# Performance work log

Measured on AMD Instinct MI355X. Metric: run time of the kernel, lower is better.

Reference implementation:

```python
import jax, jax.numpy as jnp
import numpy as np

D, HEADS, PTS, NQ, BEV_H, BEV_W, NCLS, BS, NL = 256, 8, 4, 900, 200, 200, 10, 4, 6
HD = D // HEADS
PC = (-51.2, -51.2, -5.0, 51.2, 51.2, 3.0)


def _ln(x, w, b):
    m = x.mean(-1, keepdims=True)
    v = ((x - m) ** 2).mean(-1, keepdims=True)
    return (x - m) * jax.lax.rsqrt(v + 1e-5) * w + b


def _inv_sig(x, eps=1e-5):
    x = jnp.clip(x, 0.0, 1.0)
    return jnp.log(jnp.clip(x, eps, None) / jnp.clip(1.0 - x, eps, None))


def _mha(q_in, k_in, v_in, in_w, in_b, out_w, out_b):
    # torch nn.MultiheadAttention (eval, dropout=0): packed in_proj (3D,D)
    b, n, _ = q_in.shape
    qw, kw, vw = jnp.split(in_w, 3, axis=0)
    qb, kb, vb = jnp.split(in_b, 3, axis=0)
    q = (q_in @ qw.T + qb).reshape(b, n, HEADS, HD)
    k = (k_in @ kw.T + kb).reshape(b, k_in.shape[1], HEADS, HD)
    v = (v_in @ vw.T + vb).reshape(b, v_in.shape[1], HEADS, HD)
    s = jnp.einsum('bqhd,bkhd->bhqk', q, k) * (1.0 / float(np.sqrt(HD)))
    a = jax.nn.softmax(s, axis=-1)
    o = jnp.einsum('bhqk,bkhd->bqhd', a, v).reshape(b, n, D)
    return o @ out_w.T + out_b


def _deform_attn(q, identity, value, ref2d, off_w, off_b, aw_w, aw_b, vp_w, vp_b, op_w, op_b):
    # CustomMSDeformableAttention, num_levels=1, num_points=4; bilinear grid_sample
    # semantics: align_corners=False, zero padding.
    b, n, _ = q.shape
    hw = value.shape[1]
    v = (value @ vp_w.T + vp_b).reshape(b, hw, HEADS, HD)
    vg = v.transpose(0, 2, 1, 3)  # (b, heads, HW, hd)
    off = (q @ off_w.T + off_b).reshape(b, n, HEADS, PTS, 2)
    aw = jax.nn.softmax((q @ aw_w.T + aw_b).reshape(b, n, HEADS, PTS), axis=-1)
    norm = jnp.array([BEV_W, BEV_H], jnp.float32)  # offset_normalizer = (W, H)
    loc = ref2d[:, :, None, None, :] + off / norm  # (b,n,heads,P,2) in [0,1]
    # grid_sample align_corners=False pixel coords
    x = (loc[..., 0] * BEV_W - 0.5).transpose(0, 2, 1, 3)  # (b,heads,n,P)
    y = (loc[..., 1] * BEV_H - 0.5).transpose(0, 2, 1, 3)
    x0 = jnp.floor(x); y0 = jnp.floor(y)
    x0i = x0.astype(jnp.int32); y0i = y0.astype(jnp.int32)
    fx = x - x0; fy = y - y0
    sampled = jnp.zeros(x.shape + (HD,), q.dtype)
    for dy, wy in ((0, 1.0 - fy), (1, fy)):
        for dx, wx in ((0, 1.0 - fx), (1, fx)):
            xi = x0i + dx; yi = y0i + dy
            valid = (xi >= 0) & (xi < BEV_W) & (yi >= 0) & (yi < BEV_H)
            lin = jnp.clip(yi, 0, BEV_H - 1) * BEV_W + jnp.clip(xi, 0, BEV_W - 1)
            g = jnp.take_along_axis(vg, lin.reshape(b, HEADS, n * PTS)[..., None], axis=2)
            g = g.reshape(b, HEADS, n, PTS, HD)
            sampled = sampled + g * (wx * wy * valid)[..., None]
    out = jnp.einsum('bhnpc,bnhp->bnhc', sampled, aw).reshape(b, n, D)
    return identity + (out @ op_w.T + op_b)


def _forward(bev_embed, query_embed, ref_w, ref_b, sa_in_w, sa_in_b, sa_out_w, sa_out_b,
             ln_w, ln_b, off_w, off_b, aw_w, aw_b, vproj_w, vproj_b, oproj_w, oproj_b,
             ffn_w1, ffn_b1, ffn_w2, ffn_b2, reg_w1, reg_b1, reg_w2, reg_b2, reg_w3, reg_b3,
             cls_w1, cls_b1, cls_w2, cls_b2, cls_w3, cls_b3, cls_ln_w, cls_ln_b):
    bs = bev_embed.shape[0]
    qpos = jnp.broadcast_to(query_embed[None, :, :D], (bs, NQ, D))
    q = jnp.broadcast_to(query_embed[None, :, D:], (bs, NQ, D))
    ref = jax.nn.sigmoid(qpos @ ref_w.T + ref_b)  # (bs, NQ, 3)
    init_ref = ref

    def reg_apply(i, x):
        h = jax.nn.relu(x @ reg_w1[i].T + reg_b1[i])
        h = jax.nn.relu(h @ reg_w2[i].T + reg_b2[i])
        return h @ reg_w3[i].T + reg_b3[i]

    hs, refs = [], []
    for i in range(NL):
        # self_attn -> norm
        sa = _mha(q + qpos, q + qpos, q, sa_in_w[i], sa_in_b[i], sa_out_w[i], sa_out_b[i])
        q = _ln(q + sa, ln_w[i, 0], ln_b[i, 0])
        # cross_attn (deformable) -> norm; query_pos added inside attn, identity pre-pos
        ca = _deform_attn(q + qpos, q, bev_embed, ref[..., :2], off_w[i], off_b[i],
                          aw_w[i], aw_b[i], vproj_w[i], vproj_b[i], oproj_w[i], oproj_b[i])
        q = _ln(ca, ln_w[i, 1], ln_b[i, 1])
        # ffn -> norm
        ff = jax.nn.relu(q @ ffn_w1[i].T + ffn_b1[i]) @ ffn_w2[i].T + ffn_b2[i]
        q = _ln(q + ff, ln_w[i, 2], ln_b[i, 2])
        # iterative box refinement (detached in torch)
        tmp = reg_apply(i, q)
        new_ref = jnp.concatenate([
            jax.nn.sigmoid(tmp[..., :2] + _inv_sig(ref[..., :2])),
            jax.nn.sigmoid(tmp[..., 4:5] + _inv_sig(ref[..., 2:3]))], axis=-1)
        ref = jax.lax.stop_gradient(new_ref)
        hs.append(q)
        refs.append(ref)

    cls_list, coord_list = [], []
    for i in range(NL):
        r = _inv_sig(init_ref if i == 0 else refs[i - 1])
        x = hs[i]
        h = jax.nn.relu(_ln(x @ cls_w1[i].T + cls_b1[i], cls_ln_w[i, 0], cls_ln_b[i, 0]))
        h = jax.nn.relu(_ln(h @ cls_w2[i].T + cls_b2[i], cls_ln_w[i, 1], cls_ln_b[i, 1]))
        cls = h @ cls_w3[i].T + cls_b3[i]
        tmp = reg_apply(i, x)
        xy = jax.nn.sigmoid(tmp[..., 0:2] + r[..., 0:2])
        z = jax.nn.sigmoid(tmp[..., 4:5] + r[..., 2:3])
        cx = xy[..., 0:1] * (PC[3] - PC[0]) + PC[0]
        cy = xy[..., 1:2] * (PC[4] - PC[1]) + PC[1]
        cz = z * (PC[5] - PC[2]) + PC[2]
        coord = jnp.concatenate([cx, cy, tmp[..., 2:4], cz, tmp[..., 5:]], axis=-1)
        cls_list.append(cls)
        coord_list.append(coord)
    # (NL, bs, NQ, NCLS+10): classes and boxes concatenated on last dim
    return jnp.concatenate([jnp.stack(cls_list), jnp.stack(coord_list)], axis=-1)


def setup_inputs() -> dict:
    key = jax.random.key(0)
    ks = iter(jax.random.split(key, 64))
    def nrm(shape, s=0.02):
        return jax.random.normal(next(ks), shape, jnp.float32) * s
    d, C = D, NCLS
    return dict(
        bev_embed=jax.random.normal(next(ks), (BS, BEV_H * BEV_W, d), jnp.float32),
        query_embed=nrm((NQ, 2 * d), 1.0),
        ref_w=nrm((3, d)), ref_b=jnp.zeros((3,), jnp.float32),
        sa_in_w=nrm((NL, 3 * d, d)), sa_in_b=jnp.zeros((NL, 3 * d), jnp.float32),
        sa_out_w=nrm((NL, d, d)), sa_out_b=jnp.zeros((NL, d), jnp.float32),
        ln_w=jnp.ones((NL, 3, d), jnp.float32), ln_b=jnp.zeros((NL, 3, d), jnp.float32),
        off_w=nrm((NL, HEADS * PTS * 2, d)), off_b=nrm((NL, HEADS * PTS * 2), 0.5),
        aw_w=nrm((NL, HEADS * PTS, d)), aw_b=jnp.zeros((NL, HEADS * PTS), jnp.float32),
        vproj_w=nrm((NL, d, d)), vproj_b=jnp.zeros((NL, d), jnp.float32),
        oproj_w=nrm((NL, d, d)), oproj_b=jnp.zeros((NL, d), jnp.float32),
        ffn_w1=nrm((NL, 2 * d, d)), ffn_b1=jnp.zeros((NL, 2 * d), jnp.float32),
        ffn_w2=nrm((NL, d, 2 * d)), ffn_b2=jnp.zeros((NL, d), jnp.float32),
        reg_w1=nrm((NL, d, d)), reg_b1=jnp.zeros((NL, d), jnp.float32),
        reg_w2=nrm((NL, d, d)), reg_b2=jnp.zeros((NL, d), jnp.float32),
        reg_w3=nrm((NL, 10, d)), reg_b3=jnp.zeros((NL, 10), jnp.float32),
        cls_w1=nrm((NL, d, d)), cls_b1=jnp.zeros((NL, d), jnp.float32),
        cls_w2=nrm((NL, d, d)), cls_b2=jnp.zeros((NL, d), jnp.float32),
        cls_w3=nrm((NL, C, d)), cls_b3=jnp.zeros((NL, C), jnp.float32),
        cls_ln_w=jnp.ones((NL, 2, d), jnp.float32), cls_ln_b=jnp.zeros((NL, 2, d), jnp.float32),
    )


def reference(bev_embed, query_embed, ref_w, ref_b, sa_in_w, sa_in_b, sa_out_w, sa_out_b,
              ln_w, ln_b, off_w, off_b, aw_w, aw_b, vproj_w, vproj_b, oproj_w, oproj_b,
              ffn_w1, ffn_b1, ffn_w2, ffn_b2, reg_w1, reg_b1, reg_w2, reg_b2, reg_w3, reg_b3,
              cls_w1, cls_b1, cls_w2, cls_b2, cls_w3, cls_b3, cls_ln_w, cls_ln_b):
    return _forward(bev_embed, query_embed, ref_w, ref_b, sa_in_w, sa_in_b, sa_out_w, sa_out_b,
                    ln_w, ln_b, off_w, off_b, aw_w, aw_b, vproj_w, vproj_b, oproj_w, oproj_b,
                    ffn_w1, ffn_b1, ffn_w2, ffn_b2, reg_w1, reg_b1, reg_w2, reg_b2, reg_w3, reg_b3,
                    cls_w1, cls_b1, cls_w2, cls_b2, cls_w3, cls_b3, cls_ln_w, cls_ln_b)
```

## Files before the change

kernel.cpp:

```cpp
#include <hip/hip_runtime.h>
#include <math.h>

#define DD 256
#define NQQ 900
#define NBS 4
#define NLAYER 6
#define BEVH 200
#define BEVW 200
#define ROWS (NBS*NQQ)
#define BIGN (1<<30)
#define KDEF 2080

typedef __attribute__((ext_vector_type(8))) short bf16x8;
typedef __attribute__((ext_vector_type(4))) float f32x4;

__device__ __forceinline__ float sigmoidf_(float x){ return 1.0f/(1.0f+expf(-x)); }
__device__ __forceinline__ float invsigf_(float x){
  x = fminf(fmaxf(x,0.0f),1.0f);
  float lo = fmaxf(x,1e-5f), hi = fmaxf(1.0f-x,1e-5f);
  return logf(lo/hi);
}
__device__ __forceinline__ unsigned f2bf1(float x){
  unsigned u = __float_as_uint(x);
  return (u + 0x7fffu + ((u>>16)&1u)) >> 16;
// ... 153 lines not shown
    for (int fr=0; fr<2; ++fr)
      #pragma unroll
      for (int fc=0; fc<2; ++fc) {
        const f32x4 av = fr ? (fc ? acc11 : acc10) : (fc ? acc01 : acc00);
        const int col = n0 + wc*32 + fc*16 + fm;
        const float bias = (col<N) ? ((col<NB) ? B0[col] : B1[col-NB]) : 0.0f;
        #pragma unroll
        for (int r=0; r<4; ++r)
          writeout(av[r] + bias, m0 + wr*32 + fr*16 + kb*4 + r, col);
      }
  } else {
    const int ai0 = fm*32 + ((kb^(fm&3))<<3);
    const int ai1 = (fm+16)*32 + ((kb^(fm&3))<<3);
    const int bcol = wv*16 + fm;
    const int bi = bcol*32 + ((kb^(bcol&3))<<3);
    f32x4 acc0={0,0,0,0}, acc1={0,0,0,0};
    loadg(0); writes(0); __syncthreads();
    for (int s=0; s<NS; ++s) {
      if (s+1<NS) loadg((s+1)<<5);
      const int bf = s&1;
      bf16x8 a0 = *(bf16x8*)&As[bf][ai0];
      bf16x8 a1 = *(bf16x8*)&As[bf][ai1];
      bf16x8 b  = *(bf16x8*)&Bs[bf][bi];
      acc0 = __builtin_amdgcn_mfma_f32_16x16x32_bf16(a0,b,acc0,0,0,0);
      acc1 = __builtin_amdgcn_mfma_f32_16x16x32_bf16(a1,b,acc1,0,0,0);
      if (s+1<NS) { __syncthreads(); writes((s+1)&1); __syncthreads(); }
    }
    const int col = n0 + wv*16 + fm;
    const float bias = (col<N) ? ((col<NB) ? B0[col] : B1[col-NB]) : 0.0f;
    #pragma unroll
    for (int r=0; r<4; ++r) {
      writeout(acc0[r] + bias, m0 + kb*4 + r, col);
      writeout(acc1[r] + bias, m0 + 16 + kb*4 + r, col);
    }
  }
}

__global__ __launch_bounds__(256) void attn3_k(
    const ushort* __restrict__ QKb, const ushort* __restrict__ Vb, ushort* __restrict__ Ob)
{
  const int b = blockIdx.x >> 3, h = blockIdx.x & 7;
  const int wv = threadIdx.x >> 6, lane = threadIdx.x & 63;
  const int t = threadIdx.x;
  const int qt = blockIdx.y*64 + wv*16;
  const int lq = lane & 15, lg = lane >> 4;
  const int q = qt + lq;

  __shared__ ushort Ks[2][32*40];
  __shared__ ushort Vt[2][32*34];

  bf16x8 qf = *(const bf16x8*)(QKb + (size_t)(b*NQQ + min(q, NQQ-1))*512 + h*32 + lg*8);
  f32x4 ot0 = {0.f,0.f,0.f,0.f}, ot1 = {0.f,0.f,0.f,0.f};
  float m = -3e38f, l = 0.0f;

  const ushort* kg = QKb + (size_t)b*NQQ*512 + 256 + h*32;
  const ushort* vg = Vb  + (size_t)b*NQQ*256 + h*32;
  const int srow = t>>3, sc4 = (t&7)*4;

  ushort4 kv, vv;
  auto sload = [&](int k0){
    const int gr = min(k0 + srow, NQQ-1);
    kv = *(const ushort4*)(kg + (size_t)gr*512 + sc4);
    vv = *(const ushort4*)(vg + (size_t)gr*256 + sc4);
  };
  auto swrite = [&](int bf){
    *(ushort4*)&Ks[bf][srow*40 + sc4] = kv;
    Vt[bf][(sc4+0)*34 + srow] = vv.x;
    Vt[bf][(sc4+1)*34 + srow] = vv.y;
    Vt[bf][(sc4+2)*34 + srow] = vv.z;
    Vt[bf][(sc4+3)*34 + srow] = vv.w;
// ... 48 lines not shown
    const int A1 = __builtin_amdgcn_ds_bpermute(pbase,    c01);
    const int B1 = __builtin_amdgcn_ds_bpermute(pbase,    c11);
    const int A2 = __builtin_amdgcn_ds_bpermute(pbase+64, c00);
    const int B2 = __builtin_amdgcn_ds_bpermute(pbase+64, c10);
    const int A3 = __builtin_amdgcn_ds_bpermute(pbase+64, c01);
    const int B3 = __builtin_amdgcn_ds_bpermute(pbase+64, c11);
    union { bf16x8 v; int u[4]; } pv;
    pv.u[0] = hiC ? B0 : A0; pv.u[1] = hiC ? B1 : A1;
    pv.u[2] = hiC ? B2 : A2; pv.u[3] = hiC ? B3 : A3;

    bf16x8 vf0, vf1;
    {
      union { bf16x8 v; unsigned u[4]; } u0, u1;
      const int rb = 8*lg;
      #pragma unroll
      for (int jj=0;jj<4;++jj) {
        u0.u[jj] = *(const unsigned*)&Vt[bf][lq*34 + rb + 2*jj];
        u1.u[jj] = *(const unsigned*)&Vt[bf][(16+lq)*34 + rb + 2*jj];
      }
      vf0 = u0.v; vf1 = u1.v;
    }
    ot0 = __builtin_amdgcn_mfma_f32_16x16x32_bf16(vf0, pv.v, ot0, 0, 0, 0);
    ot1 = __builtin_amdgcn_mfma_f32_16x16x32_bf16(vf1, pv.v, ot1, 0, 0, 0);
    if (c+1 < NC) { __syncthreads(); swrite((c+1)&1); __syncthreads(); }
  }
  if (q < NQQ && qt < NQQ) {
    const float inv = 1.0f / l;
    ushort* op = Ob + (size_t)(b*NQQ + q)*256 + h*32;
    uint2 w0, w1;
    w0.x = pk2(ot0[0]*inv, ot0[1]*inv); w0.y = pk2(ot0[2]*inv, ot0[3]*inv);
    w1.x = pk2(ot1[0]*inv, ot1[1]*inv); w1.y = pk2(ot1[2]*inv, ot1[3]*inv);
    *(uint2*)(op + 4*lg)      = w0;
    *(uint2*)(op + 16 + 4*lg) = w1;
  }
}

__global__ __launch_bounds__(256) void ln_k(
    const float* X, int xld, const float* R,
    const float* __restrict__ w, const float* __restrict__ b,
    float* Y, ushort* Yb, const float* qpos, ushort* Ypb, int relu)
{
  const int row = blockIdx.x*4 + (threadIdx.x>>6);
  const int lane = threadIdx.x & 63;
  if (row >= ROWS) return;
  float4 x = *(const float4*)(X + (size_t)row*xld + (lane<<2));
  if (R) { const float4 r = *(const float4*)(R + (size_t)row*256 + (lane<<2)); x.x+=r.x; x.y+=r.y; x.z+=r.z; x.w+=r.w; }
  float s = x.x+x.y+x.z+x.w;
  #pragma unroll
  for (int o=32;o>0;o>>=1) s += __shfl_xor(s,o);
  const float mean = s * (1.0f/256.0f);
  float4 d; d.x=x.x-mean; d.y=x.y-mean; d.z=x.z-mean; d.w=x.w-mean;
  float s2 = d.x*d.x+d.y*d.y+d.z*d.z+d.w*d.w;
  #pragma unroll
  for (int o=32;o>0;o>>=1) s2 += __shfl_xor(s2,o);
  const float rs = rsqrtf(s2*(1.0f/256.0f) + 1e-5f);
  const float4 wv = *(const float4*)(w + (lane<<2));
  const float4 bv = *(const float4*)(b + (lane<<2));
  float4 y;
  y.x = d.x*rs*wv.x + bv.x; y.y = d.y*rs*wv.y + bv.y;
  y.z = d.z*rs*wv.z + bv.z; y.w = d.w*rs*wv.w + bv.w;
  if (relu) { y.x=fmaxf(y.x,0.f); y.y=fmaxf(y.y,0.f); y.z=fmaxf(y.z,0.f); y.w=fmaxf(y.w,0.f); }
  if (Y)  *(float4*)(Y + (size_t)row*256 + (lane<<2)) = y;
  if (Yb) *(ushort4*)(Yb + (size_t)row*256 + (lane<<2)) = pk4(y);
  if (Ypb) {
    const float4 qp = *(const float4*)(qpos + (size_t)row*256 + (lane<<2));
    float4 zz; zz.x=y.x+qp.x; zz.y=y.y+qp.y; zz.z=y.z+qp.z; zz.w=y.w+qp.w;
    *(ushort4*)(Ypb + (size_t)row*256 + (lane<<2)) = pk4(zz);
  }
}

__global__ __launch_bounds__(512) void gather_k(
    const ushort* __restrict__ bevb, const float* __restrict__ offaw,
    const float* __restrict__ ref, ushort* __restrict__ rr)
{
  const int row = blockIdx.x;
  const int h = threadIdx.x >> 6, lane = threadIdx.x & 63;
  const int b = row / NQQ;
  const float refx = ref[row*3+0], refy = ref[row*3+1];
  const float* oa = offaw + (size_t)row*96;
  float aw[4];
  {
    const float a0=oa[64+h*4+0], a1=oa[64+h*4+1], a2=oa[64+h*4+2], a3=oa[64+h*4+3];
    const float mx = fmaxf(fmaxf(a0,a1), fmaxf(a2,a3));
    const float e0=__expf(a0-mx), e1=__expf(a1-mx), e2=__expf(a2-mx), e3=__expf(a3-mx);
    const float inv = 1.0f/(e0+e1+e2+e3);
    aw[0]=e0*inv; aw[1]=e1*inv; aw[2]=e2*inv; aw[3]=e3*inv;
  }
  float r0=0.f, r1=0.f, r2=0.f, r3=0.f, sacc=0.f;
  const ushort* bb = bevb + (size_t)b*BEVH*BEVW*DD;
  #pragma unroll
  for (int p=0;p<4;++p) {
    const float ox = oa[h*8+p*2+0], oy = oa[h*8+p*2+1];
    const float x = (refx + ox*(1.0f/BEVW))*BEVW - 0.5f;
    const float y = (refy + oy*(1.0f/BEVH))*BEVH - 0.5f;
    const float x0f = floorf(x), y0f = floorf(y);
    const int x0 = (int)x0f, y0 = (int)y0f;
    const float fx = x - x0f, fy = y - y0f;
    #pragma unroll
    for (int dy=0;dy<2;++dy) {
      #pragma unroll
// ... 36 lines not shown
  }
  __syncthreads();
  const int tx = t&15, ty = t>>4;
  float acc[4][4] = {};
  for (int j=0;j<32;++j) {
    float a[4], bv[4];
    #pragma unroll
    for (int r=0;r<4;++r) a[r] = Ao[ty*4+r][j];
    #pragma unroll
    for (int cc=0;cc<4;++cc) bv[cc] = Bo[j][tx*4+cc];
    #pragma unroll
    for (int r=0;r<4;++r)
      #pragma unroll
      for (int cc=0;cc<4;++cc) acc[r][cc] += a[r]*bv[cc];
  }
  #pragma unroll
  for (int r=0;r<4;++r)
    #pragma unroll
    for (int cc=0;cc<4;++cc)
      Wfull[((size_t)l*256 + ct*64+ty*4+r)*KDEF + h*256 + kt*64 + tx*4+cc] = (ushort)f2bf1(acc[r][cc]);
}

__global__ void wcombB_k(const float* __restrict__ opw, const float* __restrict__ vpb,
                         ushort* __restrict__ Wfull)
{
  const int l = blockIdx.x; const int c = threadIdx.x;
  ushort* wr = Wfull + ((size_t)l*256 + c)*KDEF;
  for (int h=0; h<8; ++h) {
    float s = 0.f;
    for (int j=0;j<32;++j) s += opw[(size_t)l*65536 + (size_t)c*256 + h*32+j] * vpb[l*256 + h*32+j];
    wr[2048 + h] = (ushort)f2bf1(s);
  }
  for (int zz=2056; zz<KDEF; ++zz) wr[zz] = 0;
}

__global__ __launch_bounds__(256) void regcls3_k(
    const float* __restrict__ rc2,
    const float* __restrict__ lnw, const float* __restrict__ lnb,
    const float* __restrict__ rw3, const float* __restrict__ rb3,
    const float* __restrict__ cw3, const float* __restrict__ cb3,
    float* __restrict__ ref, float* __restrict__ outL)
{
  __shared__ float Wr[10*272];
  __shared__ float Wc[10*272];
  for (int i=threadIdx.x; i<2560; i+=256) {
    const int o = i>>8, k = i&255;
    const int si = o*272 + (k>>6)*68 + (k&63);
    Wr[si] = rw3[i]; Wc[si] = cw3[i];
  }
  __syncthreads();
  const int t = threadIdx.x;
  const int row = t>>3, g = (t>>2)&1, sl = t&3;
  const int R = blockIdx.x*32 + row;
  const bool act = R < ROWS;
  const float* base = rc2 + (size_t)(act?R:0)*512 + g*256 + sl*64;
  float4 v[16];
  #pragma unroll
  for (int jj=0;jj<16;++jj) v[jj] = *(const float4*)(base + 4*jj);
  float s1 = 0.f, s2 = 0.f;
  #pragma unroll
  for (int jj=0;jj<16;++jj) {
    s1 += v[jj].x+v[jj].y+v[jj].z+v[jj].w;
    s2 += v[jj].x*v[jj].x+v[jj].y*v[jj].y+v[jj].z*v[jj].z+v[jj].w*v[jj].w;
  }
  s1 += __shfl_xor(s1,1); s1 += __shfl_xor(s1,2);
  s2 += __shfl_xor(s2,1); s2 += __shfl_xor(s2,2);
  if (g) {
    const float mean = s1*(1.0f/256.0f);
    const float var = s2*(1.0f/256.0f) - mean*mean;
    const float rs = rsqrtf(var + 1e-5f);
    #pragma unroll
    for (int jj=0;jj<16;++jj) {
      const float4 w4 = *(const float4*)(lnw + sl*64 + 4*jj);
      const float4 b4 = *(const float4*)(lnb + sl*64 + 4*jj);
      v[jj].x = fmaxf((v[jj].x-mean)*rs*w4.x + b4.x, 0.f);
      v[jj].y = fmaxf((v[jj].y-mean)*rs*w4.y + b4.y, 0.f);
      v[jj].z = fmaxf((v[jj].z-mean)*rs*w4.z + b4.z, 0.f);
      v[jj].w = fmaxf((v[jj].w-mean)*rs*w4.w + b4.w, 0.f);
    }
  }
  const float* Wg = g ? Wc : Wr;
  float acc[10] = {};
  #pragma unroll
  for (int jj=0;jj<16;++jj) {
    #pragma unroll
    for (int o=0;o<10;++o) {
      const float4 w = *(const float4*)&Wg[o*272 + sl*68 + 4*jj];
      acc[o] += v[jj].x*w.x + v[jj].y*w.y + v[jj].z*w.z + v[jj].w*w.w;
    }
  }
  #pragma unroll
  for (int o=0;o<10;++o) {
    acc[o] += __shfl_xor(acc[o], 1);
    acc[o] += __shfl_xor(acc[o], 2);
  }
  if (act && sl == 0) {
    if (g) {
      float* oc = outL + (size_t)R*20;
      #pragma unroll
      for (int o=0;o<10;++o) oc[o] = acc[o] + cb3[o];
    } else {
      float tt[10];
      #pragma unroll
      for (int o=0;o<10;++o) tt[o] = acc[o] + rb3[o];
      const float rx = invsigf_(ref[R*3+0]);
      const float ry = invsigf_(ref[R*3+1]);
      const float rz = invsigf_(ref[R*3+2]);
      const float nx = sigmoidf_(tt[0]+rx);
      const float ny = sigmoidf_(tt[1]+ry);
      const float nz = sigmoidf_(tt[4]+rz);
      ref[R*3+0]=nx; ref[R*3+1]=ny; ref[R*3+2]=nz;
      float* o = outL + (size_t)R*20 + 10;
      o[0]=nx*102.4f-51.2f; o[1]=ny*102.4f-51.2f; o[2]=tt[2]; o[3]=tt[3];
      o[4]=nz*8.0f-5.0f; o[5]=tt[5]; o[6]=tt[6]; o[7]=tt[7]; o[8]=tt[8]; o[9]=tt[9];
    }
  }
}

__global__ void init_k(const float* __restrict__ qe, float* __restrict__ qpos,
                       float* __restrict__ q, ushort* __restrict__ qb, ushort* __restrict__ qpb)
{
  const int t = blockIdx.x*blockDim.x + threadIdx.x;
  const int row = t >> 6; const int cc = (t & 63) << 2;
  const int n = row % NQQ;
  const float4 vp = *(const float4*)(qe + (size_t)n*512 + cc);
  const float4 vq = *(const float4*)(qe + (size_t)n*512 + 256 + cc);
  *(float4*)(qpos + (size_t)row*256 + cc) = vp;
  *(float4*)(q    + (size_t)row*256 + cc) = vq;
  *(ushort4*)(qb  + (size_t)row*256 + cc) = pk4(vq);
  float4 s; s.x=vq.x+vp.x; s.y=vq.y+vp.y; s.z=vq.z+vp.z; s.w=vq.w+vp.w;
  *(ushort4*)(qpb + (size_t)row*256 + cc) = pk4(s);
}

__global__ void prep_k(const float* __restrict__ ow, const float* __restrict__ ob,
                       const float* __restrict__ aw, const float* __restrict__ ab,
                       const float* __restrict__ rw, const float* __restrict__ rb,
                       const float* __restrict__ cw, const float* __restrict__ cb,
                       ushort* cwAb, float* cbA, ushort* cwBb, float* cbB)
{
  const int i = blockIdx.x*blockDim.x + threadIdx.x;
  if (i < 6*96*256) {
    const int l = i/(96*256), r = (i/256)%96, k = i%256;
    const float v = (r<64) ? ow[((size_t)l*64 + r)*256 + k] : aw[((size_t)l*32 + (r-64))*256 + k];
    cwAb[i] = (ushort)f2bf1(v);
  }
  if (i < 576) { const int l = i/96, r = i%96; cbA[i] = (r<64) ? ob[l*64+r] : ab[l*32 + r-64]; }
  if (i < 6*512*256) {
    const int l = i/(512*256), r = (i/256)%512, k = i%256;
    const float v = (r<256) ? rw[((size_t)l*256+r)*256+k] : cw[((size_t)l*256 + (r-256))*256 + k];
// ... 59 lines not shown
  const float* reg_w1   = (const float*)d_in[22];
  const float* reg_b1   = (const float*)d_in[23];
  const float* reg_w2   = (const float*)d_in[24];
  const float* reg_b2   = (const float*)d_in[25];
  const float* reg_w3   = (const float*)d_in[26];
  const float* reg_b3   = (const float*)d_in[27];
  const float* cls_w1   = (const float*)d_in[28];
  const float* cls_b1   = (const float*)d_in[29];
  const float* cls_w2   = (const float*)d_in[30];
  const float* cls_b2   = (const float*)d_in[31];
  const float* cls_w3   = (const float*)d_in[32];
  const float* cls_b3   = (const float*)d_in[33];
  const float* cls_ln_w = (const float*)d_in[34];
  const float* cls_ln_b = (const float*)d_in[35];
  float* out = (float*)d_out;

  float* ws    = (float*)d_ws;
  float* qpos  = ws;
  float* q     = qpos + 921600;
  float* tA    = q    + 921600;
  float* tB    = tA   + 921600;
  float* rc2   = tB   + 921600;
  float* cls1f = rc2  + 1843200;
  float* offaw = cls1f+ 921600;
  float* ref   = offaw+ 345600;
  float* cbA   = ref  + 10800;
  float* cbB   = cbA  + 576;
  ushort* usb  = (ushort*)(ws + 6811248);
  ushort* rr   = usb;
  ushort* QKb  = usb;
  ushort* Vb   = usb + 1843200;
  ushort* tAb  = usb + 2764800;
  ushort* W5b  = usb + 3686400;
  ushort* clsb = usb + 5529600;
  ushort* regb = usb + 6451200;
  ushort* qb   = usb + 7488000;
  ushort* qpb  = usb + 8409600;
  ushort* bevb = usb + 9331200;
  ushort* wbf  = usb + 50291200;
  ushort* siwb = wbf;
  ushort* sowb = wbf + 1179648;
  ushort* f1wb = wbf + 1966080;
  ushort* f2wb = wbf + 2752512;
  ushort* r2wb = wbf + 3538944;
  ushort* c2wb = wbf + 3932160;
  ushort* cwAb = wbf + 4325376;
  ushort* cwBb = wbf + 4472832;
  ushort* Wfull= wbf + 5259264;

  auto G = [&](int BM, const ushort* A0, const ushort* A1, int NA, int lda,
               const ushort* W0, const ushort* W1, int NW,
               const float* B0, const float* B1, int NB,
               void* Y0, int ldy0, int obf0,
               void* Y1, int ldy1, int obf1, int NY,
               int M, int N, int K, int reluN) {
    dim3 grid((M+BM-1)/BM, (N+63)/64);
    if (BM==64)
      gemmb_k<64><<<grid, 256, 0, stream>>>(A0,A1,NA,lda,W0,W1,NW,B0,B1,NB,
                                            Y0,ldy0,obf0,Y1,ldy1,obf1,NY,M,N,K,reluN);
    else
      gemmb_k<32><<<grid, 256, 0, stream>>>(A0,A1,NA,lda,W0,W1,NW,B0,B1,NB,
                                            Y0,ldy0,obf0,Y1,ldy1,obf1,NY,M,N,K,reluN);
  };

  cvtbev_k<<<20000, 256, 0, stream>>>(bev, bevb);
  cvtw_k<<<4224, 256, 0, stream>>>(sa_in_w, sa_out_w, oproj_w, ffn_w1, ffn_w2, reg_w2, cls_w2, wbf);
  prep_k<<<3072, 256, 0, stream>>>(off_w, off_b, aw_w, aw_b, reg_w1, reg_b1, cls_w1, cls_b1,
                                   cwAb, cbA, cwBb, cbB);
  wcomb_k<<<dim3(16,8,6), 256, 0, stream>>>(oproj_w, vproj_w, Wfull);
  wcombB_k<<<6, 256, 0, stream>>>(oproj_w, vproj_b, Wfull);
  init_k<<<900, 256, 0, stream>>>(qe, qpos, q, qb, qpb);
  {
    dim3 grid((ROWS+63)/64, 1);
    gemm_k<<<grid, 256, 0, stream>>>(qpos, 256, ref_w, ref_b, ref, ROWS, 3, 256, 3, 2);
  }

  for (int i=0;i<NLAYER;++i) {
    const float* sib = sa_in_b + (size_t)i*768;
    const ushort* siw = siwb + (size_t)i*196608;
    G(64, qpb, qb, 512, 256, siw, siw, BIGN, sib, sib, BIGN,
      QKb, 512, 1, Vb, 256, 1, 512, ROWS, 768, 256, 0);
    attn3_k<<<dim3(32,15), 256, 0, stream>>>(QKb, Vb, tAb);
    G(32, tAb, tAb, BIGN, 256, sowb + (size_t)i*65536, nullptr, BIGN,
      sa_out_b + (size_t)i*256, nullptr, BIGN,
      tB, 256, 0, nullptr, 0, 0, BIGN, ROWS, 256, 256, 0);
    ln_k<<<900, 256, 0, stream>>>(tB, 256, q, ln_w + (size_t)(i*3+0)*256, ln_b + (size_t)(i*3+0)*256,
                                  q, nullptr, qpos, qpb, 0);
    G(32, qpb, qpb, BIGN, 256, cwAb + (size_t)i*24576, nullptr, BIGN,
      cbA + i*96, nullptr, BIGN,
      offaw, 96, 0, nullptr, 0, 0, BIGN, ROWS, 96, 256, 0);
    gather_k<<<ROWS, 512, 0, stream>>>(bevb, offaw, ref, rr);
    G(32, rr, rr, BIGN, KDEF, Wfull + (size_t)i*256*KDEF, nullptr, BIGN,
      oproj_b + (size_t)i*256, nullptr, BIGN,
      tA, 256, 0, nullptr, 0, 0, BIGN, ROWS, 256, KDEF, 0);
    ln_k<<<900, 256, 0, stream>>>(tA, 256, q, ln_w + (size_t)(i*3+1)*256, ln_b + (size_t)(i*3+1)*256,
                                  q, qb, nullptr, nullptr, 0);
    G(64, qb, qb, BIGN, 256, f1wb + (size_t)i*131072, nullptr, BIGN,
      ffn_b1 + (size_t)i*512, nullptr, BIGN,
      W5b, 512, 1, nullptr, 0, 0, BIGN, ROWS, 512, 256, 512);
    G(32, W5b, W5b, BIGN, 512, f2wb + (size_t)i*131072, nullptr, BIGN,
      ffn_b2 + (size_t)i*256, nullptr, BIGN,
      tA, 256, 0, nullptr, 0, 0, BIGN, ROWS, 256, 512, 0);
    ln_k<<<900, 256, 0, stream>>>(tA, 256, q, ln_w + (size_t)(i*3+2)*256, ln_b + (size_t)(i*3+2)*256,
                                  q, qb, qpos, qpb, 0);
    G(64, qb, qb, BIGN, 256, cwBb + (size_t)i*131072, nullptr, BIGN,
      cbB + i*512, nullptr, BIGN,
      regb, 256, 1, cls1f, 256, 0, 256, ROWS, 512, 256, 256);
    ln_k<<<900, 256, 0, stream>>>(cls1f, 256, nullptr,
                                  cls_ln_w + (size_t)(i*2+0)*256, cls_ln_b + (size_t)(i*2+0)*256,
                                  nullptr, clsb, nullptr, nullptr, 1);
    G(64, regb, clsb, 256, 256,
      r2wb + (size_t)i*65536, c2wb + (size_t)i*65536, 256,
      reg_b2 + (size_t)i*256, cls_b2 + (size_t)i*256, 256,
      rc2, 512, 0, nullptr, 0, 0, BIGN, ROWS, 512, 256, 256);
    regcls3_k<<<(ROWS+31)/32, 256, 0, stream>>>(rc2,
        cls_ln_w + (size_t)(i*2+1)*256, cls_ln_b + (size_t)(i*2+1)*256,
        reg_w3 + (size_t)i*2560, reg_b3 + (size_t)i*10,
        cls_w3 + (size_t)i*2560, cls_b3 + (size_t)i*10,
        ref, out + (size_t)i*ROWS*20);
  }
}
```

Before: 1.169 ms.

## Fuse output GEMMs with residual-add LayerNorm in full-row kernels

Adds a templated fullrow_k kernel. Each block computes all output columns for 16 rows with bf16 MFMA, staging the accumulators in shared memory. It then applies bias, residual add, LayerNorm and optional ReLU, and writes the fp32, bf16 and bf16+qpos outputs directly. This replaces four GEMM + ln_k pairs per layer, which removes the separate LN launches and the fp32 intermediate round trips. In exchange, only 225 blocks are launched and every block streams the whole weight matrix, including the K=2080 deformable projection, so weight traffic per block rises and parallelism drops. Variance is now computed as E[x²]−mean², which is less numerically stable than the old two-pass form.

Measured after the change: 1.262 ms. 8.0% more time.

```diff
diff --git a/kernel.cpp b/kernel.cpp
--- a/kernel.cpp
+++ b/kernel.cpp
@@ -213,6 +213,155 @@
   }
 }
 
+template<int BN, int MODE>
+__global__ __launch_bounds__(256) void fullrow_k(
+    const ushort* __restrict__ A, int lda, const ushort* __restrict__ W,
+    const float* __restrict__ bias,
+    const float* __restrict__ R, const float* __restrict__ lnw, const float* __restrict__ lnb,
+    float* __restrict__ Yq, ushort* __restrict__ Yb,
+    const float* __restrict__ qpos, ushort* __restrict__ Ypb,
+    ushort* __restrict__ regb, ushort* __restrict__ clsb, int K)
+{
+  constexpr int P   = (MODE==0) ? 260 : 516;
+  constexpr int SMG = BN*64 + 1024;
+  constexpr int SME = 16*P*4;
+  constexpr int SMB = (SMG > SME) ? SMG : SME;
+  __shared__ char smraw[SMB];
+  ushort* Ws = (ushort*)smraw;
+  ushort* As = ((ushort*)smraw) + BN*32;
+  float*  Ep = (float*)smraw;
+
+  const int t = threadIdx.x;
+  const int m0 = blockIdx.x*16;
+  const int wv = t>>6, lane = t&63;
+  const int fm = lane&15, kb = lane>>4;
+  constexpr int NF = BN/64;
+  constexpr int WR = BN/256;
+  const int colbase = wv*(BN/4);
+  const int NS = K>>5;
+
+  const int arow = t>>2, ak = t&3;
+  const ushort* ap = A + (size_t)(m0+arow)*lda + ak*8;
+
+  bf16x8 pa; bf16x8 pw[WR*4];
+  auto loadr = [&](int c){
+    if (t < 64) pa = *(const bf16x8*)(ap + c*32);
+    #pragma unroll
+    for (int rr2=0; rr2<WR; ++rr2) {
+      const ushort* wp = W + (size_t)(t + rr2*256)*K + c*32;
+      #pragma unroll
+      for (int j=0;j<4;++j) pw[rr2*4+j] = *(const bf16x8*)(wp + j*8);
+    }
+  };
+  auto stores = [&](){
+    if (t < 64) *(bf16x8*)&As[arow*32 + ((ak ^ (arow&3))<<3)] = pa;
+    #pragma unroll
+    for (int rr2=0; rr2<WR; ++rr2) {
+      const int wr = t + rr2*256;
+      #pragma unroll
+      for (int j=0;j<4;++j)
+        *(bf16x8*)&Ws[wr*32 + ((j ^ (wr&3))<<3)] = pw[rr2*4+j];
+    }
+  };
+
+  f32x4 acc[NF];
+  #pragma unroll
+  for (int f=0;f<NF;++f) acc[f] = (f32x4){0,0,0,0};
+
+  loadr(0); stores(); __syncthreads();
+  for (int s=0; s<NS; ++s) {
+    if (s+1<NS) loadr(s+1);
+    bf16x8 af = *(bf16x8*)&As[fm*32 + ((kb ^ (fm&3))<<3)];
+    #pragma unroll
+    for (int f=0;f<NF;++f) {
+      const int col = colbase + f*16 + fm;
+      bf16x8 bfv = *(bf16x8*)&Ws[col*32 + ((kb ^ (col&3))<<3)];
+      acc[f] = __builtin_amdgcn_mfma_f32_16x16x32_bf16(af, bfv, acc[f], 0, 0, 0);
+    }
+    __syncthreads();
+    if (s+1<NS) { stores(); __syncthreads(); }
+  }
+
+  #pragma unroll
+  for (int f=0;f<NF;++f) {
+    const int col = colbase + f*16 + fm;
+    const float bs = bias[col];
+    #pragma unroll
+    for (int r=0;r<4;++r) Ep[(kb*4+r)*P + col] = acc[f][r] + bs;
+  }
+  __syncthreads();
+
+  const int row = t>>4, cg = t&15;
+  const int gr = m0 + row;
+  if constexpr (MODE==0) {
+    float x[16];
+    float s1 = 0.f, s2 = 0.f;
+    const float* rp = R + (size_t)gr*256 + cg*16;
+    #pragma unroll
+    for (int j=0;j<16;j+=4) {
+      float4 e = *(float4*)&Ep[row*P + cg*16 + j];
+      const float4 rv = *(const float4*)(rp + j);
+      x[j]=e.x+rv.x; x[j+1]=e.y+rv.y; x[j+2]=e.z+rv.z; x[j+3]=e.w+rv.w;
+      s1 += x[j]+x[j+1]+x[j+2]+x[j+3];
+      s2 += x[j]*x[j]+x[j+1]*x[j+1]+x[j+2]*x[j+2]+x[j+3]*x[j+3];
+    }
+    s1 += __shfl_xor(s1,1); s1 += __shfl_xor(s1,2); s1 += __shfl_xor(s1,4); s1 += __shfl_xor(s1,8);
+    s2 += __shfl_xor(s2,1); s2 += __shfl_xor(s2,2); s2 += __shfl_xor(s2,4); s2 += __shfl_xor(s2,8);
+    const float mean = s1*(1.0f/256.0f);
+    const float var  = s2*(1.0f/256.0f) - mean*mean;
+    const float rs   = rsqrtf(var + 1e-5f);
+    #pragma unroll
+    for (int j=0;j<16;j+=4) {
+      const float4 w4 = *(const float4*)(lnw + cg*16 + j);
+      const float4 b4 = *(const float4*)(lnb + cg*16 + j);
+      float4 y;
+      y.x = (x[j+0]-mean)*rs*w4.x + b4.x;
+      y.y = (x[j+1]-mean)*rs*w4.y + b4.y;
+      y.z = (x[j+2]-mean)*rs*w4.z + b4.z;
+      y.w = (x[j+3]-mean)*rs*w4.w + b4.w;
+      *(float4*)&Yq[(size_t)gr*256 + cg*16 + j] = y;
+      if (Yb) *(ushort4*)&Yb[(size_t)gr*256 + cg*16 + j] = pk4(y);
+      if (Ypb) {
+        const float4 qp = *(const float4*)(qpos + (size_t)gr*256 + cg*16 + j);
+        float4 z; z.x=y.x+qp.x; z.y=y.y+qp.y; z.z=y.z+qp.z; z.w=y.w+qp.w;
+        *(ushort4*)&Ypb[(size_t)gr*256 + cg*16 + j] = pk4(z);
+      }
+    }
+  } else {
+    #pragma unroll
+    for (int j=0;j<16;j+=4) {
+      float4 e = *(float4*)&Ep[row*P + cg*16 + j];
+      e.x=fmaxf(e.x,0.f); e.y=fmaxf(e.y,0.f); e.z=fmaxf(e.z,0.f); e.w=fmaxf(e.w,0.f);
+      *(ushort4*)&regb[(size_t)gr*256 + cg*16 + j] = pk4(e);
+    }
+    float x[16];
+    float s1 = 0.f, s2 = 0.f;
+    #pragma unroll
+    for (int j=0;j<16;j+=4) {
+      const float4 e = *(float4*)&Ep[row*P + 256 + cg*16 + j];
+      x[j]=e.x; x[j+1]=e.y; x[j+2]=e.z; x[j+3]=e.w;
+      s1 += e.x+e.y+e.z+e.w;
+      s2 += e.x*e.x+e.y*e.y+e.z*e.z+e.w*e.w;
+    }
+    s1 += __shfl_xor(s1,1); s1 += __shfl_xor(s1,2); s1 += __shfl_xor(s1,4); s1 += __shfl_xor(s1,8);
+    s2 += __shfl_xor(s2,1); s2 += __shfl_xor(s2,2); s2 += __shfl_xor(s2,4); s2 += __shfl_xor(s2,8);
+    const float mean = s1*(1.0f/256.0f);
+    const float var  = s2*(1.0f/256.0f) - mean*mean;
+    const float rs   = rsqrtf(var + 1e-5f);
+    #pragma unroll
+    for (int j=0;j<16;j+=4) {
+      const float4 w4 = *(const float4*)(lnw + cg*16 + j);
+      const float4 b4 = *(const float4*)(lnb + cg*16 + j);
+      float4 y;
+      y.x = fmaxf((x[j+0]-mean)*rs*w4.x + b4.x, 0.f);
+      y.y = fmaxf((x[j+1]-mean)*rs*w4.y + b4.y, 0.f);
+      y.z = fmaxf((x[j+2]-mean)*rs*w4.z + b4.z, 0.f);
+      y.w = fmaxf((x[j+3]-mean)*rs*w4.w + b4.w, 0.f);
+      *(ushort4*)&clsb[(size_t)gr*256 + cg*16 + j] = pk4(y);
+    }
+  }
+}
+
 __global__ __launch_bounds__(256) void attn3_k(
     const ushort* __restrict__ QKb, const ushort* __restrict__ Vb, ushort* __restrict__ Ob)
 {
@@ -327,40 +476,6 @@
     w1.x = pk2(ot1[0]*inv, ot1[1]*inv); w1.y = pk2(ot1[2]*inv, ot1[3]*inv);
     *(uint2*)(op + 4*lg)      = w0;
     *(uint2*)(op + 16 + 4*lg) = w1;
-  }
-}
-
-__global__ __launch_bounds__(256) void ln_k(
-    const float* X, int xld, const float* R,
-    const float* __restrict__ w, const float* __restrict__ b,
-    float* Y, ushort* Yb, const float* qpos, ushort* Ypb, int relu)
-{
-  const int row = blockIdx.x*4 + (threadIdx.x>>6);
-  const int lane = threadIdx.x & 63;
-  if (row >= ROWS) return;
-  float4 x = *(const float4*)(X + (size_t)row*xld + (lane<<2));
-  if (R) { const float4 r = *(const float4*)(R + (size_t)row*256 + (lane<<2)); x.x+=r.x; x.y+=r.y; x.z+=r.z; x.w+=r.w; }
-  float s = x.x+x.y+x.z+x.w;
-  #pragma unroll
-  for (int o=32;o>0;o>>=1) s += __shfl_xor(s,o);
-  const float mean = s * (1.0f/256.0f);
-  float4 d; d.x=x.x-mean; d.y=x.y-mean; d.z=x.z-mean; d.w=x.w-mean;
-  float s2 = d.x*d.x+d.y*d.y+d.z*d.z+d.w*d.w;
-  #pragma unroll
-  for (int o=32;o>0;o>>=1) s2 += __shfl_xor(s2,o);
-  const float rs = rsqrtf(s2*(1.0f/256.0f) + 1e-5f);
-  const float4 wv = *(const float4*)(w + (lane<<2));
-  const float4 bv = *(const float4*)(b + (lane<<2));
-  float4 y;
-  y.x = d.x*rs*wv.x + bv.x; y.y = d.y*rs*wv.y + bv.y;
-  y.z = d.z*rs*wv.z + bv.z; y.w = d.w*rs*wv.w + bv.w;
-  if (relu) { y.x=fmaxf(y.x,0.f); y.y=fmaxf(y.y,0.f); y.z=fmaxf(y.z,0.f); y.w=fmaxf(y.w,0.f); }
-  if (Y)  *(float4*)(Y + (size_t)row*256 + (lane<<2)) = y;
-  if (Yb) *(ushort4*)(Yb + (size_t)row*256 + (lane<<2)) = pk4(y);
-  if (Ypb) {
-    const float4 qp = *(const float4*)(qpos + (size_t)row*256 + (lane<<2));
-    float4 zz; zz.x=y.x+qp.x; zz.y=y.y+qp.y; zz.z=y.z+qp.z; zz.w=y.w+qp.w;
-    *(ushort4*)(Ypb + (size_t)row*256 + (lane<<2)) = pk4(zz);
   }
 }
 
@@ -720,34 +835,29 @@
     G(64, qpb, qb, 512, 256, siw, siw, BIGN, sib, sib, BIGN,
       QKb, 512, 1, Vb, 256, 1, 512, ROWS, 768, 256, 0);
     attn3_k<<<dim3(32,15), 256, 0, stream>>>(QKb, Vb, tAb);
-    G(32, tAb, tAb, BIGN, 256, sowb + (size_t)i*65536, nullptr, BIGN,
-      sa_out_b + (size_t)i*256, nullptr, BIGN,
-      tB, 256, 0, nullptr, 0, 0, BIGN, ROWS, 256, 256, 0);
-    ln_k<<<900, 256, 0, stream>>>(tB, 256, q, ln_w + (size_t)(i*3+0)*256, ln_b + (size_t)(i*3+0)*256,
-                                  q, nullptr, qpos, qpb, 0);
+    fullrow_k<256,0><<<225, 256, 0, stream>>>(
+        tAb, 256, sowb + (size_t)i*65536, sa_out_b + (size_t)i*256,
+        q, ln_w + (size_t)(i*3+0)*256, ln_b + (size_t)(i*3+0)*256,
+        q, nullptr, qpos, qpb, nullptr, nullptr, 256);
     G(32, qpb, qpb, BIGN, 256, cwAb + (size_t)i*24576, nullptr, BIGN,
       cbA + i*96, nullptr, BIGN,
       offaw, 96, 0, nullptr, 0, 0, BIGN, ROWS, 96, 256, 0);
     gather_k<<<ROWS, 512, 0, stream>>>(bevb, offaw, ref, rr);
-    G(32, rr, rr, BIGN, KDEF, Wfull + (size_t)i*256*KDEF, nullptr, BIGN,
-      oproj_b + (size_t)i*256, nullptr, BIGN,
-      tA, 256, 0, nullptr, 0, 0, BIGN, ROWS, 256, KDEF, 0);
-    ln_k<<<900, 256, 0, stream>>>(tA, 256, q, ln_w + (size_t)(i*3+1)*256, ln_b + (size_t)(i*3+1)*256,
-                                  q, qb, nullptr, nullptr, 0);
+    fullrow_k<256,0><<<225, 256, 0, stream>>>(
+        rr, KDEF, Wfull + (size_t)i*256*KDEF, oproj_b + (size_t)i*256,
+        q, ln_w + (size_t)(i*3+1)*256, ln_b + (size_t)(i*3+1)*256,
+        q, qb, nullptr, nullptr, nullptr, nullptr, KDEF);
     G(64, qb, qb, BIGN, 256, f1wb + (size_t)i*131072, nullptr, BIGN,
       ffn_b1 + (size_t)i*512, nullptr, BIGN,
       W5b, 512, 1, nullptr, 0, 0, BIGN, ROWS, 512, 256, 512);
-    G(32, W5b, W5b, BIGN, 512, f2wb + (size_t)i*131072, nullptr, BIGN,
-      ffn_b2 + (size_t)i*256, nullptr, BIGN,
-      tA, 256, 0, nullptr, 0, 0, BIGN, ROWS, 256, 512, 0);
-    ln_k<<<900, 256, 0, stream>>>(tA, 256, q, ln_w + (size_t)(i*3+2)*256, ln_b + (size_t)(i*3+2)*256,
-                                  q, qb, qpos, qpb, 0);
-    G(64, qb, qb, BIGN, 256, cwBb + (size_t)i*131072, nullptr, BIGN,
-      cbB + i*512, nullptr, BIGN,
-      regb, 256, 1, cls1f, 256, 0, 256, ROWS, 512, 256, 256);
-    ln_k<<<900, 256, 0, stream>>>(cls1f, 256, nullptr,
-                                  cls_ln_w + (size_t)(i*2+0)*256, cls_ln_b + (size_t)(i*2+0)*256,
-                                  nullptr, clsb, nullptr, nullptr, 1);
+    fullrow_k<256,0><<<225, 256, 0, stream>>>(
+        W5b, 512, f2wb + (size_t)i*131072, ffn_b2 + (size_t)i*256,
+        q, ln_w + (size_t)(i*3+2)*256, ln_b + (size_t)(i*3+2)*256,
+        q, qb, qpos, qpb, nullptr, nullptr, 512);
+    fullrow_k<512,1><<<225, 256, 0, stream>>>(
+        qb, 256, cwBb + (size_t)i*131072, cbB + i*512,
+        nullptr, cls_ln_w + (size_t)(i*2+0)*256, cls_ln_b + (size_t)(i*2+0)*256,
+        nullptr, nullptr, nullptr, nullptr, regb, clsb, 256);
     G(64, regb, clsb, 256, 256,
       r2wb + (size_t)i*65536, c2wb + (size_t)i*65536, 256,
       reg_b2 + (size_t)i*256, cls_b2 + (size_t)i*256, 256,
```

## Fuse reg/cls branch MLP heads and final projection into one tail kernel

Applied to the files above, without the earlier changes.

Replaces the per-layer sequence of two GEMM launches, a LayerNorm launch and the regcls3 kernel with a single tail_k that processes 16 rows per block. The first layer, ReLU or LayerNorm+ReLU, the second layer and the final 10-wide projections with reference-point update all run in shared memory. This removes three launches per layer and the global round trips of regb, clsb, cls1f and rc2. In exchange only 225 blocks of 16 rows are launched, and each block re-streams the full weight matrices from global through a small shared tile with many syncs, which may underuse the MFMA units and the GPU's compute units.

Measured after the change: 1.339 ms. 14.6% more time.

```diff
diff --git a/kernel.cpp b/kernel.cpp
--- a/kernel.cpp
+++ b/kernel.cpp
@@ -209,6 +209,217 @@
     for (int r=0; r<4; ++r) {
       writeout(acc0[r] + bias, m0 + kb*4 + r, col);
       writeout(acc1[r] + bias, m0 + 16 + kb*4 + r, col);
+    }
+  }
+}
+
+__global__ __launch_bounds__(256) void tail_k(
+    const ushort* __restrict__ qb,
+    const ushort* __restrict__ w1, const float* __restrict__ b1,
+    const float* __restrict__ ln1w, const float* __restrict__ ln1b,
+    const ushort* __restrict__ w2r, const ushort* __restrict__ w2c,
+    const float* __restrict__ b2r, const float* __restrict__ b2c,
+    const float* __restrict__ ln2w, const float* __restrict__ ln2b,
+    const float* __restrict__ rw3, const float* __restrict__ rb3,
+    const float* __restrict__ cw3, const float* __restrict__ cb3,
+    float* __restrict__ ref, float* __restrict__ outL)
+{
+  __shared__ ushort As_[16*264];
+  __shared__ ushort Ws_[64*128];
+  __shared__ ushort Ar_[16*256];
+  __shared__ ushort Ac_[16*256];
+  __shared__ float  Hc_[16*264];
+
+  const int t = threadIdx.x;
+  const int m0 = blockIdx.x*16;
+  const int wv = t>>6, lane = t&63;
+  const int fm = lane&15, kb = lane>>4;
+  const int colL = wv*16 + fm;
+
+  {
+    const int row = t>>4, seg = t&15;
+    const ushort* ap = qb + (size_t)(m0+row)*256 + seg*16;
+    #pragma unroll
+    for (int j=0;j<2;++j) {
+      bf16x8 v = *(const bf16x8*)(ap + j*8);
+      const int k = seg*16 + j*8;
+      *(bf16x8*)&As_[row*264 + ((k>>5)<<5) + ((((k>>3)&3)^(row&3))<<3)] = v;
+    }
+  }
+  __syncthreads();
+
+  for (int chunk=0; chunk<8; ++chunk) {
+    f32x4 acc = {0,0,0,0};
+    for (int kc=0; kc<2; ++kc) {
+      __syncthreads();
+      for (int i=t; i<1024; i+=256) {
+        const int r = i>>4, kl = (i&15)*8;
+        bf16x8 v = *(const bf16x8*)(w1 + (size_t)(chunk*64+r)*256 + kc*128 + kl);
+        *(bf16x8*)&Ws_[r*128 + ((kl>>5)<<5) + ((((kl>>3)&3)^(r&3))<<3)] = v;
+      }
+      __syncthreads();
+      #pragma unroll
+      for (int s=0;s<4;++s) {
+        const int st = kc*4 + s;
+        bf16x8 af  = *(bf16x8*)&As_[fm*264 + (st<<5) + ((kb^(fm&3))<<3)];
+        bf16x8 bfv = *(bf16x8*)&Ws_[colL*128 + (s<<5) + ((kb^(colL&3))<<3)];
+        acc = __builtin_amdgcn_mfma_f32_16x16x32_bf16(af, bfv, acc, 0,0,0);
+      }
+    }
+    const int gcol = chunk*64 + colL;
+    const float bias = b1[gcol];
+    #pragma unroll
+    for (int r=0;r<4;++r) {
+      const int row = kb*4 + r;
+      float v = acc[r] + bias;
+      if (chunk < 4) {
+        v = fmaxf(v, 0.0f);
+        Ar_[row*256 + ((gcol>>5)<<5) + ((((gcol>>3)&3)^(row&3))<<3) + (gcol&7)] = (ushort)f2bf1(v);
+      } else {
+        Hc_[row*264 + (gcol-256)] = v;
+      }
+    }
+  }
+  __syncthreads();
+
+  {
+    const int row = t>>4, cg = t&15;
+    float x[16]; float s1=0.f, s2=0.f;
+    #pragma unroll
+    for (int j=0;j<16;j+=4) {
+      float4 e = *(float4*)&Hc_[row*264 + cg*16 + j];
+      x[j]=e.x; x[j+1]=e.y; x[j+2]=e.z; x[j+3]=e.w;
+      s1 += e.x+e.y+e.z+e.w;
+      s2 += e.x*e.x+e.y*e.y+e.z*e.z+e.w*e.w;
+    }
+    s1 += __shfl_xor(s1,1); s1 += __shfl_xor(s1,2); s1 += __shfl_xor(s1,4); s1 += __shfl_xor(s1,8);
+    s2 += __shfl_xor(s2,1); s2 += __shfl_xor(s2,2); s2 += __shfl_xor(s2,4); s2 += __shfl_xor(s2,8);
+    const float mean = s1*(1.0f/256.0f);
+    const float var  = s2*(1.0f/256.0f) - mean*mean;
+    const float rs   = rsqrtf(var + 1e-5f);
+    #pragma unroll
+    for (int jj=0;jj<2;++jj) {
+      const int k0 = cg*16 + jj*8;
+      union { bf16x8 v; unsigned u[4]; } uu;
+      #pragma unroll
+      for (int p=0;p<4;++p) {
+        const int j = jj*8 + p*2;
+        const float w0 = ln1w[k0 + p*2],     b0 = ln1b[k0 + p*2];
+        const float w1v = ln1w[k0 + p*2 + 1], b1v = ln1b[k0 + p*2 + 1];
+        const float y0 = fmaxf((x[j]-mean)*rs*w0 + b0, 0.0f);
+        const float y1 = fmaxf((x[j+1]-mean)*rs*w1v + b1v, 0.0f);
+        uu.u[p] = pk2(y0, y1);
+      }
+      *(bf16x8*)&Ac_[row*256 + ((k0>>5)<<5) + ((((k0>>3)&3)^(row&3))<<3)] = uu.v;
+    }
+  }
+  __syncthreads();
+
+  for (int chunk=0; chunk<8; ++chunk) {
+    const ushort* Wsrc = (chunk<4) ? w2r : w2c;
+    const int wrb = (chunk&3)*64;
+    f32x4 acc = {0,0,0,0};
+    for (int kc=0; kc<2; ++kc) {
+      __syncthreads();
+      for (int i=t; i<1024; i+=256) {
+        const int r = i>>4, kl = (i&15)*8;
+        bf16x8 v = *(const bf16x8*)(Wsrc + (size_t)(wrb+r)*256 + kc*128 + kl);
+        *(bf16x8*)&Ws_[r*128 + ((kl>>5)<<5) + ((((kl>>3)&3)^(r&3))<<3)] = v;
+      }
+      __syncthreads();
+      #pragma unroll
+      for (int s=0;s<4;++s) {
+        const int st = kc*4 + s;
+        const ushort* Asrc = (chunk<4) ? Ar_ : Ac_;
+        bf16x8 af  = *(bf16x8*)&Asrc[fm*256 + (st<<5) + ((kb^(fm&3))<<3)];
+        bf16x8 bfv = *(bf16x8*)&Ws_[colL*128 + (s<<5) + ((kb^(colL&3))<<3)];
+        acc = __builtin_amdgcn_mfma_f32_16x16x32_bf16(af, bfv, acc, 0,0,0);
+      }
+    }
+    const int gcol2 = wrb + colL;
+    const float bias = (chunk<4) ? b2r[gcol2] : b2c[gcol2];
+    #pragma unroll
+    for (int r=0;r<4;++r) {
+      const int row = kb*4 + r;
+      float v = acc[r] + bias;
+      if (chunk < 4) {
+        v = fmaxf(v, 0.0f);
+        As_[row*264 + gcol2] = (ushort)f2bf1(v);
+      } else {
+        Hc_[row*264 + gcol2] = v;
+      }
+    }
+  }
+  __syncthreads();
+
+  {
+    const int row = t>>4, sub = t&15;
+    const int g = sub>>3, sl = sub&7;
+    const int R = m0 + row;
+    float x[32];
+    if (g == 0) {
+      #pragma unroll
+      for (int j=0;j<32;j+=4) {
+        ushort4 u = *(ushort4*)&As_[row*264 + sl*32 + j];
+        x[j]=bf2f(u.x); x[j+1]=bf2f(u.y); x[j+2]=bf2f(u.z); x[j+3]=bf2f(u.w);
+      }
+    } else {
+      float s1=0.f, s2=0.f;
+      #pragma unroll
+      for (int j=0;j<32;j+=4) {
+        float4 e = *(float4*)&Hc_[row*264 + sl*32 + j];
+        x[j]=e.x; x[j+1]=e.y; x[j+2]=e.z; x[j+3]=e.w;
+        s1 += e.x+e.y+e.z+e.w;
+        s2 += e.x*e.x+e.y*e.y+e.z*e.z+e.w*e.w;
+      }
+      s1 += __shfl_xor(s1,1); s1 += __shfl_xor(s1,2); s1 += __shfl_xor(s1,4);
+      s2 += __shfl_xor(s2,1); s2 += __shfl_xor(s2,2); s2 += __shfl_xor(s2,4);
+      const float mean = s1*(1.0f/256.0f);
+      const float var  = s2*(1.0f/256.0f) - mean*mean;
+      const float rs   = rsqrtf(var + 1e-5f);
+      #pragma unroll
+      for (int j=0;j<32;++j) {
+        const int k = sl*32 + j;
+        x[j] = fmaxf((x[j]-mean)*rs*ln2w[k] + ln2b[k], 0.0f);
+      }
+    }
+    const float* W3 = g ? cw3 : rw3;
+    float acc[10] = {};
+    #pragma unroll
+    for (int o=0;o<10;++o) {
+      const float* wp = W3 + o*256 + sl*32;
+      #pragma unroll
+      for (int j=0;j<32;j+=4) {
+        const float4 w = *(const float4*)(wp + j);
+        acc[o] += x[j]*w.x + x[j+1]*w.y + x[j+2]*w.z + x[j+3]*w.w;
+      }
+    }
+    #pragma unroll
+    for (int o=0;o<10;++o) {
+      acc[o] += __shfl_xor(acc[o],1);
+      acc[o] += __shfl_xor(acc[o],2);
+      acc[o] += __shfl_xor(acc[o],4);
+    }
+    if (sl == 0) {
+      if (g) {
+        float* oc = outL + (size_t)R*20;
+        #pragma unroll
+        for (int o=0;o<10;++o) oc[o] = acc[o] + cb3[o];
+      } else {
+        float tt[10];
+        #pragma unroll
+        for (int o=0;o<10;++o) tt[o] = acc[o] + rb3[o];
+        const float rx = invsigf_(ref[R*3+0]);
+        const float ry = invsigf_(ref[R*3+1]);
+        const float rz = invsigf_(ref[R*3+2]);
+        const float nx = sigmoidf_(tt[0]+rx);
+        const float ny = sigmoidf_(tt[1]+ry);
+        const float nz = sigmoidf_(tt[4]+rz);
+        ref[R*3+0]=nx; ref[R*3+1]=ny; ref[R*3+2]=nz;
+        float* o = outL + (size_t)R*20 + 10;
+        o[0]=nx*102.4f-51.2f; o[1]=ny*102.4f-51.2f; o[2]=tt[2]; o[3]=tt[3];
+        o[4]=nz*8.0f-5.0f; o[5]=tt[5]; o[6]=tt[6]; o[7]=tt[7]; o[8]=tt[8]; o[9]=tt[9];
+      }
     }
   }
 }
@@ -463,89 +674,6 @@
     wr[2048 + h] = (ushort)f2bf1(s);
   }
   for (int zz=2056; zz<KDEF; ++zz) wr[zz] = 0;
-}
-
-__global__ __launch_bounds__(256) void regcls3_k(
-    const float* __restrict__ rc2,
-    const float* __restrict__ lnw, const float* __restrict__ lnb,
-    const float* __restrict__ rw3, const float* __restrict__ rb3,
-    const float* __restrict__ cw3, const float* __restrict__ cb3,
-    float* __restrict__ ref, float* __restrict__ outL)
-{
-  __shared__ float Wr[10*272];
-  __shared__ float Wc[10*272];
-  for (int i=threadIdx.x; i<2560; i+=256) {
-    const int o = i>>8, k = i&255;
-    const int si = o*272 + (k>>6)*68 + (k&63);
-    Wr[si] = rw3[i]; Wc[si] = cw3[i];
-  }
-  __syncthreads();
-  const int t = threadIdx.x;
-  const int row = t>>3, g = (t>>2)&1, sl = t&3;
-  const int R = blockIdx.x*32 + row;
-  const bool act = R < ROWS;
-  const float* base = rc2 + (size_t)(act?R:0)*512 + g*256 + sl*64;
-  float4 v[16];
-  #pragma unroll
-  for (int jj=0;jj<16;++jj) v[jj] = *(const float4*)(base + 4*jj);
-  float s1 = 0.f, s2 = 0.f;
-  #pragma unroll
-  for (int jj=0;jj<16;++jj) {
-    s1 += v[jj].x+v[jj].y+v[jj].z+v[jj].w;
-    s2 += v[jj].x*v[jj].x+v[jj].y*v[jj].y+v[jj].z*v[jj].z+v[jj].w*v[jj].w;
-  }
-  s1 += __shfl_xor(s1,1); s1 += __shfl_xor(s1,2);
-  s2 += __shfl_xor(s2,1); s2 += __shfl_xor(s2,2);
-  if (g) {
-    const float mean = s1*(1.0f/256.0f);
-    const float var = s2*(1.0f/256.0f) - mean*mean;
-    const float rs = rsqrtf(var + 1e-5f);
-    #pragma unroll
-    for (int jj=0;jj<16;++jj) {
-      const float4 w4 = *(const float4*)(lnw + sl*64 + 4*jj);
-      const float4 b4 = *(const float4*)(lnb + sl*64 + 4*jj);
-      v[jj].x = fmaxf((v[jj].x-mean)*rs*w4.x + b4.x, 0.f);
-      v[jj].y = fmaxf((v[jj].y-mean)*rs*w4.y + b4.y, 0.f);
-      v[jj].z = fmaxf((v[jj].z-mean)*rs*w4.z + b4.z, 0.f);
-      v[jj].w = fmaxf((v[jj].w-mean)*rs*w4.w + b4.w, 0.f);
-    }
-  }
-  const float* Wg = g ? Wc : Wr;
-  float acc[10] = {};
-  #pragma unroll
-  for (int jj=0;jj<16;++jj) {
-    #pragma unroll
-    for (int o=0;o<10;++o) {
-      const float4 w = *(const float4*)&Wg[o*272 + sl*68 + 4*jj];
-      acc[o] += v[jj].x*w.x + v[jj].y*w.y + v[jj].z*w.z + v[jj].w*w.w;
-    }
-  }
-  #pragma unroll
-  for (int o=0;o<10;++o) {
-    acc[o] += __shfl_xor(acc[o], 1);
-    acc[o] += __shfl_xor(acc[o], 2);
-  }
-  if (act && sl == 0) {
-    if (g) {
-      float* oc = outL + (size_t)R*20;
-      #pragma unroll
-      for (int o=0;o<10;++o) oc[o] = acc[o] + cb3[o];
-    } else {
-      float tt[10];
-      #pragma unroll
-      for (int o=0;o<10;++o) tt[o] = acc[o] + rb3[o];
-      const float rx = invsigf_(ref[R*3+0]);
-      const float ry = invsigf_(ref[R*3+1]);
-      const float rz = invsigf_(ref[R*3+2]);
-      const float nx = sigmoidf_(tt[0]+rx);
-      const float ny = sigmoidf_(tt[1]+ry);
-      const float nz = sigmoidf_(tt[4]+rz);
-      ref[R*3+0]=nx; ref[R*3+1]=ny; ref[R*3+2]=nz;
-      float* o = outL + (size_t)R*20 + 10;
-      o[0]=nx*102.4f-51.2f; o[1]=ny*102.4f-51.2f; o[2]=tt[2]; o[3]=tt[3];
-      o[4]=nz*8.0f-5.0f; o[5]=tt[5]; o[6]=tt[6]; o[7]=tt[7]; o[8]=tt[8]; o[9]=tt[9];
-    }
-  }
 }
 
 __global__ void init_k(const float* __restrict__ qe, float* __restrict__ qpos,
@@ -671,8 +799,6 @@
   ushort* Vb   = usb + 1843200;
   ushort* tAb  = usb + 2764800;
   ushort* W5b  = usb + 3686400;
-  ushort* clsb = usb + 5529600;
-  ushort* regb = usb + 6451200;
   ushort* qb   = usb + 7488000;
   ushort* qpb  = usb + 8409600;
   ushort* bevb = usb + 9331200;
@@ -742,17 +868,11 @@
       tA, 256, 0, nullptr, 0, 0, BIGN, ROWS, 256, 512, 0);
     ln_k<<<900, 256, 0, stream>>>(tA, 256, q, ln_w + (size_t)(i*3+2)*256, ln_b + (size_t)(i*3+2)*256,
                                   q, qb, qpos, qpb, 0);
-    G(64, qb, qb, BIGN, 256, cwBb + (size_t)i*131072, nullptr, BIGN,
-      cbB + i*512, nullptr, BIGN,
-      regb, 256, 1, cls1f, 256, 0, 256, ROWS, 512, 256, 256);
-    ln_k<<<900, 256, 0, stream>>>(cls1f, 256, nullptr,
-                                  cls_ln_w + (size_t)(i*2+0)*256, cls_ln_b + (size_t)(i*2+0)*256,
-                                  nullptr, clsb, nullptr, nullptr, 1);
-    G(64, regb, clsb, 256, 256,
-      r2wb + (size_t)i*65536, c2wb + (size_t)i*65536, 256,
-      reg_b2 + (size_t)i*256, cls_b2 + (size_t)i*256, 256,
-      rc2, 512, 0, nullptr, 0, 0, BIGN, ROWS, 512, 256, 256);
-    regcls3_k<<<(ROWS+31)/32, 256, 0, stream>>>(rc2,
+    tail_k<<<225, 256, 0, stream>>>(qb,
+        cwBb + (size_t)i*131072, cbB + i*512,
+        cls_ln_w + (size_t)(i*2+0)*256, cls_ln_b + (size_t)(i*2+0)*256,
+        r2wb + (size_t)i*65536, c2wb + (size_t)i*65536,
+        reg_b2 + (size_t)i*256, cls_b2 + (size_t)i*256,
         cls_ln_w + (size_t)(i*2+1)*256, cls_ln_b + (size_t)(i*2+1)*256,
         reg_w3 + (size_t)i*2560, reg_b3 + (size_t)i*10,
         cls_w3 + (size_t)i*2560, cls_b3 + (size_t)i*10,
```
